# Kernel optimization log

Hardware: AMD Instinct MI355X
Metric: run time of the kernel (lower is better)

The kernel has to match this reference:

```python
import jax, jax.numpy as jnp
import numpy as np

N_NODES = 100000
N_EDGES = 1600000
N_FEAT = 128
HIDDEN = 128
OUT = 1
NUM_GRAPHS = 2048


def setup_inputs() -> dict:
    key = jax.random.key(0)
    ks = jax.random.split(key, 8)
    x = jax.random.normal(ks[0], (N_NODES, N_FEAT), dtype=jnp.float32)
    edge_index = jax.random.randint(ks[1], (2, N_EDGES), 0, N_NODES, dtype=jnp.int64)
    batch = jnp.sort(jax.random.randint(ks[2], (N_NODES,), 0, NUM_GRAPHS, dtype=jnp.int64))
    s = 1.0 / np.sqrt(N_FEAT)
    W1 = jax.random.normal(ks[3], (N_FEAT, HIDDEN), dtype=jnp.float32) * s
    b1 = jnp.zeros((HIDDEN,), dtype=jnp.float32)
    W2 = jax.random.normal(ks[4], (HIDDEN, HIDDEN), dtype=jnp.float32) * s
    b2 = jnp.zeros((HIDDEN,), dtype=jnp.float32)
    Wlin = jax.random.normal(ks[5], (HIDDEN, OUT), dtype=jnp.float32) * s
    blin = jnp.zeros((OUT,), dtype=jnp.float32)
    return {"x": x, "edge_index": edge_index, "batch": batch,
            "W1": W1, "b1": b1, "W2": W2, "b2": b2, "Wlin": Wlin, "blin": blin}


def gcn_conv(x, W, b, src, dst, n_nodes):
    # PyG GCNConv: x' = D^{-1/2} (A + I) D^{-1/2} (X W) + b, deg includes self-loop
    xw = x @ W  # [N, H]
    deg = jax.ops.segment_sum(jnp.ones(src.shape[0], xw.dtype), dst, num_segments=n_nodes) + 1.0
    dinv = jax.lax.rsqrt(deg)
    norm = dinv[src] * dinv[dst]  # [E]
    agg = jax.ops.segment_sum(xw[src] * norm[:, None], dst, num_segments=n_nodes)
    # self-loop contribution: norm = deg^{-1}
    return agg + xw * (1.0 / deg)[:, None] + b


def global_mean_pool(x, batch, num_graphs):
    sums = jax.ops.segment_sum(x, batch, num_segments=num_graphs)
    cnts = jax.ops.segment_sum(jnp.ones(x.shape[0], x.dtype), batch, num_segments=num_graphs)
    return sums / jnp.maximum(cnts, 1.0)[:, None]


def reference(x, edge_index, batch, W1, b1, W2, b2, Wlin, blin):
    src, dst = edge_index[0], edge_index[1]
    n = x.shape[0]
    h = gcn_conv(x, W1, b1, src, dst, n)
    h = jax.nn.relu(h)  # dropout is a no-op in eval mode
    h = gcn_conv(h, W2, b2, src, dst, n)
    g = global_mean_pool(h, batch, NUM_GRAPHS)  # [G, H]
    return g @ Wlin + blin
```

## Files before the change

### kernel.cpp

```cpp
#include <hip/hip_runtime.h>

#define N_NODES   100000
#define N_EDGES   1600000
#define NFEAT     128
#define NGRAPHS   2048
#define CBSHIFT   7
#define BSZ       128
#define NCB       ((N_NODES + BSZ - 1) / BSZ)
#define N_META    (NCB * BSZ)
#define CAP       2432
#define P1_EPB    8192
#define P1_BLOCKS ((N_EDGES + P1_EPB - 1) / P1_EPB)
#define GEMM_HALF   391
#define G1_BLOCKS 2048
#define G2_BLOCKS ((4 * N_META + 255) / 256)
#define ZCNT      (NGRAPHS + NCB)
#define ZB        ((ZCNT + 255) / 256)
#define MISC_BLOCKS (17 + ZB + 8)

typedef __attribute__((ext_vector_type(8))) short short8;
typedef __attribute__((ext_vector_type(4))) float f32x4;

__device__ __forceinline__ unsigned short f2bf(float f) {
    unsigned int u = __float_as_uint(f);
    u += 0x7FFFu + ((u >> 16) & 1u);
    return (unsigned short)(u >> 16);
}

__device__ __forceinline__ void acc8s(float* acc, uint4 v, float s) {
    acc[0] = fmaf(s, __uint_as_float(v.x << 16), acc[0]);
    acc[1] = fmaf(s, __uint_as_float(v.x & 0xFFFF0000u), acc[1]);
    acc[2] = fmaf(s, __uint_as_float(v.y << 16), acc[2]);
    acc[3] = fmaf(s, __uint_as_float(v.y & 0xFFFF0000u), acc[3]);
    acc[4] = fmaf(s, __uint_as_float(v.z << 16), acc[4]);
    acc[5] = fmaf(s, __uint_as_float(v.z & 0xFFFF0000u), acc[5]);
    acc[6] = fmaf(s, __uint_as_float(v.w << 16), acc[6]);
    acc[7] = fmaf(s, __uint_as_float(v.w & 0xFFFF0000u), acc[7]);
}

__device__ __forceinline__ void gemm_tile(const float* __restrict__ X,
                                          const unsigned short* __restrict__ WT,
                                          unsigned short* __restrict__ C,
                                          int gblk, int tid) {
    const int R0   = gblk * 128;
    const int wv   = tid >> 6;
    const int lane = tid & 63;
    const int m16  = lane & 15;
    const int quad = lane >> 4;
    const int r0 = R0 + wv * 32 + m16;
    const int r1 = r0 + 16;
    const bool ok0 = r0 < N_NODES, ok1 = r1 < N_NODES;

    f32x4 acc[2][8] = {};
    #pragma unroll
    for (int ks = 0; ks < 4; ++ks) {
        const int k0 = ks * 32 + quad * 8;
        short8 a0 = {}, a1 = {};
        if (ok0) {
            float4 f0 = *(const float4*)(X + (size_t)r0 * NFEAT + k0);
            float4 f1 = *(const float4*)(X + (size_t)r0 * NFEAT + k0 + 4);
            a0[0] = (short)f2bf(f0.x); a0[1] = (short)f2bf(f0.y);
            a0[2] = (short)f2bf(f0.z); a0[3] = (short)f2bf(f0.w);
            a0[4] = (short)f2bf(f1.x); a0[5] = (short)f2bf(f1.y);
            a0[6] = (short)f2bf(f1.z); a0[7] = (short)f2bf(f1.w);
        }
        if (ok1) {
            float4 f0 = *(const float4*)(X + (size_t)r1 * NFEAT + k0);
            float4 f1 = *(const float4*)(X + (size_t)r1 * NFEAT + k0 + 4);
            a1[0] = (short)f2bf(f0.x); a1[1] = (short)f2bf(f0.y);
            a1[2] = (short)f2bf(f0.z); a1[3] = (short)f2bf(f0.w);
            a1[4] = (short)f2bf(f1.x); a1[5] = (short)f2bf(f1.y);
            a1[6] = (short)f2bf(f1.z); a1[7] = (short)f2bf(f1.w);
        }
        #pragma unroll
        for (int ct = 0; ct < 8; ++ct) {
            short8 bb = *(const short8*)(WT + (ct * 16 + m16) * 128 + k0);
            acc[0][ct] = __builtin_amdgcn_mfma_f32_16x16x32_bf16(a0, bb, acc[0][ct], 0, 0, 0);
            acc[1][ct] = __builtin_amdgcn_mfma_f32_16x16x32_bf16(a1, bb, acc[1][ct], 0, 0, 0);
        }
    }
    #pragma unroll
    for (int t2 = 0; t2 < 2; ++t2) {
        int rbase = R0 + wv * 32 + t2 * 16 + quad * 4;
        #pragma unroll
        for (int reg = 0; reg < 4; ++reg) {
            int gr = rbase + reg;
            if (gr < N_NODES) {
                #pragma unroll
                for (int ct = 0; ct < 8; ++ct)
                    C[(size_t)gr * NFEAT + ct * 16 + m16] = f2bf(acc[t2][ct][reg]);
            }
        }
    }
}

__global__ __launch_bounds__(256) void k_misc(const float* __restrict__ W1,
                                              unsigned short* __restrict__ WT1,
                                              const float* __restrict__ W2,
                                              const float* __restrict__ Wlin,
                                              const float* __restrict__ b2,
                                              const float* __restrict__ blin,
                                              float* __restrict__ w2l,
                                              int* __restrict__ zeros,
                                              const int* __restrict__ batch,
                                              float* __restrict__ cntf) {
    const int blk = blockIdx.x;
    const int t = threadIdx.x;
    if (blk < 16) {
        int base = blk * 1024 + t * 4;
        #pragma unroll
        for (int q = 0; q < 4; ++q) {
            int i = base + q;
            int n = i >> 7, k = i & 127;
            WT1[i] = f2bf(W1[k * 128 + n]);
        }
    } else if (blk == 16) {
        __shared__ float s[256];
        int i = t >> 1, half = t & 1;
        float ps = 0.f;
        for (int j = half * 64; j < half * 64 + 64; ++j)
            ps += W2[i * 128 + j] * Wlin[j];
        s[t] = ps;
        __syncthreads();
        if (!half) w2l[i] = s[t] + s[t + 1];
        __syncthreads();
        float pc = (t < 128) ? b2[t] * Wlin[t] : 0.f;
        s[t] = pc;
        __syncthreads();
        for (int off = 128; off > 0; off >>= 1) {
            if (t < off) s[t] += s[t + off];
            __syncthreads();
        }
        if (t == 0) w2l[128] = s[0] + blin[0];
    } else if (blk < 17 + ZB) {
        int i = (blk - 17) * 256 + t;
        if (i < ZCNT) zeros[i] = 0;
    } else {
        int g = (blk - (17 + ZB)) * 256 + t;
        int lo = 0, hi = N_NODES;
        while (lo < hi) { int m = (lo + hi) >> 1; if (batch[m] < g) lo = m + 1; else hi = m; }
        int lb = lo;
        lo = 0; hi = N_NODES;
        int g1 = g + 1;
        while (lo < hi) { int m = (lo + hi) >> 1; if (batch[m] < g1) lo = m + 1; else hi = m; }
        cntf[g] = fmaxf((float)(lo - lb), 1.0f);
    }
}

__global__ __launch_bounds__(256) void k_gA_p1(const float* __restrict__ X,
                                               const unsigned short* __restrict__ WT,
                                               unsigned short* __restrict__ C,
                                               const int* __restrict__ src,
                                               const int* __restrict__ dst,
                                               int* __restrict__ bcur,
                                               unsigned int* __restrict__ pairs) {
    if (blockIdx.x < GEMM_HALF) {
        gemm_tile(X, WT, C, blockIdx.x, threadIdx.x);
        return;
    }
    const int b = blockIdx.x - GEMM_HALF;
    __shared__ int hist[NCB], base[NCB], cur[NCB];
    const int t = threadIdx.x;
    for (int i = t; i < NCB; i += 256) { hist[i] = 0; cur[i] = 0; }
    __syncthreads();
    const int e0 = b * P1_EPB;
    const int e1 = min(e0 + P1_EPB, N_EDGES);
    for (int e = e0 + t; e < e1; e += 256)
        atomicAdd(&hist[dst[e] >> CBSHIFT], 1);
    __syncthreads();
    const int off0 = (b * 89) % NCB;
    for (int k = t; k < NCB; k += 256) {
        int i = k + off0;
        if (i >= NCB) i -= NCB;
        int c = hist[i];
        base[i] = c ? (i * CAP + atomicAdd(&bcur[i], c)) : 0;
    }
    __syncthreads();
    for (int e = e0 + t; e < e1; e += 256) {
        int d = dst[e];
        int bb = d >> CBSHIFT;
        int r = atomicAdd(&cur[bb], 1);
        int idx = base[bb] + r;
        if (idx < (bb + 1) * CAP)
            pairs[idx] = (unsigned int)src[e] | ((unsigned int)(d & (BSZ - 1)) << 17);
    }
}

__global__ __launch_bounds__(256) void k_gB_p2(const float* __restrict__ X,
                                               const unsigned short* __restrict__ WT,
                                               unsigned short* __restrict__ C,
                                               const unsigned int* __restrict__ pairs,
                                               const int* __restrict__ bcur,
                                               int* __restrict__ csr_src,
                                               float* __restrict__ dinv,
                                               int4* __restrict__ meta) {
    if (blockIdx.x < GEMM_HALF) {
        gemm_tile(X, WT, C, blockIdx.x + GEMM_HALF, threadIdx.x);
        return;
    }
    const int b = blockIdx.x - GEMM_HALF;
    __shared__ int hist[BSZ], sst[BSZ], cur[BSZ], s[BSZ], dh[64], dhc[64];
    const int t = threadIdx.x;
    const int beg = b * CAP;
    const int end = beg + min(bcur[b], CAP);
    if (t < BSZ) { hist[t] = 0; cur[t] = 0; }
    if (t < 64) { dh[t] = 0; dhc[t] = 0; }
    __syncthreads();
    for (int i = beg + t; i < end; i += 256)
        atomicAdd(&hist[pairs[i] >> 17], 1);
    __syncthreads();
    int v = (t < BSZ) ? hist[t] : 0;
    if (t < BSZ) s[t] = v;
    __syncthreads();
    for (int off = 1; off < BSZ; off <<= 1) {
        int x = (t >= off && t < BSZ) ? s[t - off] : 0;
        __syncthreads();
        if (t < BSZ) s[t] += x;
        __syncthreads();
    }
    if (t < BSZ) sst[t] = s[t] - v;
    __syncthreads();
    const int node = (b << CBSHIFT) + t;
    const bool valid = (t < BSZ) && (node < N_NODES);
    if (valid) {
        dinv[node] = rsqrtf((float)v + 1.0f);
        atomicAdd(&dh[63 - min(v, 63)], 1);
    }
    for (int i = beg + t; i < end; i += 256) {
        unsigned int pv = pairs[i];
        int dl = pv >> 17;
        int r = atomicAdd(&cur[dl], 1);
        csr_src[beg + sst[dl] + r] = (int)(pv & 0x1FFFFu);
    }
    __syncthreads();
    if (t < 64) s[t] = dh[t];
    __syncthreads();
    for (int off = 1; off < 64; off <<= 1) {
        int x = (t >= off && t < 64) ? s[t - off] : 0;
        __syncthreads();
        if (t < 64) s[t] += x;
        __syncthreads();
    }
    if (valid) {
        int bin = 63 - min(v, 63);
        int r = atomicAdd(&dhc[bin], 1);
        int rank = s[bin] - dh[bin] + r;
        meta[(size_t)rank * NCB + b] =
            make_int4(beg + sst[t], v, __float_as_int(rsqrtf((float)v + 1.0f)), node);
    } else if (t < BSZ) {
        meta[(size_t)t * NCB + b] = make_int4(0, 0, 0, -1);
    }
}

__global__ __launch_bounds__(256) void k_gather1(const unsigned short* __restrict__ xwb,
                                                 const int* __restrict__ csr_src,
                                                 const float* __restrict__ dinv,
                                                 const float* __restrict__ b,
                                                 const float* __restrict__ w2l,
                                                 const int4* __restrict__ meta,
                                                 float* __restrict__ z) {
    const int t     = threadIdx.x;
    const int lane  = t & 63;
    const int p     = lane & 15;
    const int gbase = lane & 48;
    const int j0    = p & 7;
    const int ngroups = G1_BLOCKS * 16;
    int gid = blockIdx.x * 16 + (t >> 4);
    const uint4* tab = (const uint4*)xwb;
    float4 b0 = *(const float4*)(b + p * 8);
    float4 b1 = *(const float4*)(b + p * 8 + 4);
    float4 w0 = *(const float4*)(w2l + p * 8);
    float4 w1 = *(const float4*)(w2l + p * 8 + 4);

    for (int nidx = gid; nidx < N_META; nidx += ngroups) {
        const int4 md = meta[nidx];
        const int node  = md.w;
        if (node < 0) continue;
        const int beg   = md.x;
        const int cnt   = md.y;
        const float dvn = __int_as_float(md.z);
        float acc[8] = {};
        acc8s(acc, tab[(size_t)node * 16 + p], dvn);
        const int nch = (cnt + 7) >> 3;
        if (nch) {
            int myA; float dvA; uint4 vA[8];
            int myB; float dvB; uint4 vB[8];
            {
                bool vld = j0 < cnt;
                int jj = vld ? j0 : 0;
                int sld = csr_src[beg + jj];
                myA = vld ? sld : node;
                float dv = dinv[myA];
                dvA = vld ? dv : 0.f;
                #pragma unroll
                for (int q = 0; q < 8; ++q) {
                    int idx = __shfl(myA, gbase + q);
                    vA[q] = tab[(size_t)idx * 16 + p];
                }
            }
            int c = 0;
            for (;;) {
                const bool hb = (c + 1 < nch);
                if (hb) {
                    int j = (c + 1) * 8 + j0;
                    bool vld = j < cnt;
                    int jj = vld ? j : 0;
                    int sld = csr_src[beg + jj];
                    myB = vld ? sld : node;
                    float dv = dinv[myB];
                    dvB = vld ? dv : 0.f;
                    #pragma unroll
                    for (int q = 0; q < 8; ++q) {
                        int idx = __shfl(myB, gbase + q);
                        vB[q] = tab[(size_t)idx * 16 + p];
                    }
                }
                #pragma unroll
                for (int q = 0; q < 8; ++q) {
                    float sv = __shfl(dvA, gbase + q);
                    acc8s(acc, vA[q], sv);
                }
                ++c;
                if (!hb) break;
                const bool ha = (c + 1 < nch);
                if (ha) {
                    int j = (c + 1) * 8 + j0;
                    bool vld = j < cnt;
                    int jj = vld ? j : 0;
                    int sld = csr_src[beg + jj];
                    myA = vld ? sld : node;
                    float dv = dinv[myA];
                    dvA = vld ? dv : 0.f;
                    #pragma unroll
                    for (int q = 0; q < 8; ++q) {
                        int idx = __shfl(myA, gbase + q);
                        vA[q] = tab[(size_t)idx * 16 + p];
                    }
                }
                #pragma unroll
                for (int q = 0; q < 8; ++q) {
                    float sv = __shfl(dvB, gbase + q);
                    acc8s(acc, vB[q], sv);
                }
                ++c;
                if (!ha) break;
            }
        }
        float s = fmaxf(acc[0] * dvn + b0.x, 0.f) * w0.x
                + fmaxf(acc[1] * dvn + b0.y, 0.f) * w0.y
                + fmaxf(acc[2] * dvn + b0.z, 0.f) * w0.z
                + fmaxf(acc[3] * dvn + b0.w, 0.f) * w0.w
                + fmaxf(acc[4] * dvn + b1.x, 0.f) * w1.x
                + fmaxf(acc[5] * dvn + b1.y, 0.f) * w1.y
                + fmaxf(acc[6] * dvn + b1.z, 0.f) * w1.z
                + fmaxf(acc[7] * dvn + b1.w, 0.f) * w1.w;
        s += __shfl_xor(s, 1);
        s += __shfl_xor(s, 2);
        s += __shfl_xor(s, 4);
        s += __shfl_xor(s, 8);
        if (p == 0) z[node] = s * dvn;
    }
}

__global__ __launch_bounds__(256) void k_g2(const float* __restrict__ z,
                                            const int* __restrict__ csr_src,
                                            const int4* __restrict__ meta,
                                            const int* __restrict__ batch,
                                            float* __restrict__ gsum) {
    int tid = blockIdx.x * blockDim.x + threadIdx.x;
    int nidx = tid >> 2;
    int q = tid & 3;
    if (nidx >= N_META) return;
    int4 md = meta[nidx];
    const int node = md.w;
    if (node < 0) return;
    const int beg = md.x, cnt = md.y;
    const float dvn = __int_as_float(md.z);
    float a = (q == 0) ? z[node] : 0.f;
    for (int j = q; j < cnt; j += 4)
        a += z[csr_src[beg + j]];
    a += __shfl_xor(a, 1);
    a += __shfl_xor(a, 2);
    if (q == 0) atomicAdd(&gsum[batch[node]], a * dvn);
}

__global__ void k_final(const float* __restrict__ gsum, const float* __restrict__ cntf,
                        const float* __restrict__ c2, float* __restrict__ out) {
    int g = blockIdx.x * blockDim.x + threadIdx.x;
    if (g >= NGRAPHS) return;
    out[g] = gsum[g] / cntf[g] + c2[0];
}

extern "C" void kernel_launch(void* const* d_in, const int* in_sizes, int n_in,
                              void* d_out, int out_size, void* d_ws, size_t ws_size,
                              hipStream_t stream) {
    const float* x    = (const float*)d_in[0];
    const int*   ei   = (const int*)d_in[1];
    const int*   bat  = (const int*)d_in[2];
    const float* W1   = (const float*)d_in[3];
    const float* b1   = (const float*)d_in[4];
    const float* W2   = (const float*)d_in[5];
    const float* b2   = (const float*)d_in[6];
    const float* Wlin = (const float*)d_in[7];
    const float* blin = (const float*)d_in[8];
    float* out = (float*)d_out;

    const int* src = ei;
    const int* dst = ei + N_EDGES;

    const size_t NF = (size_t)N_NODES * NFEAT;
    unsigned short* bufA = (unsigned short*)d_ws;
    float* z       = (float*)(bufA + NF);
    float* dinv    = z + N_NODES;
    float* gsum    = dinv + N_NODES;
    int* bcur      = (int*)(gsum + NGRAPHS);
    float* cntf    = (float*)(bcur + NCB);
    unsigned short* WT1 = (unsigned short*)(cntf + NGRAPHS);
    float* w2l     = (float*)(WT1 + 128 * 128);
    unsigned int* pairs = (unsigned int*)(w2l + 132);
    int* csr_src   = (int*)(pairs + (size_t)NCB * CAP);
    int4* meta     = (int4*)(((size_t)(csr_src + (size_t)NCB * CAP) + 15) & ~(size_t)15);

    const int BS = 256;

    k_misc<<<MISC_BLOCKS, BS, 0, stream>>>(W1, WT1, W2, Wlin, b2, blin, w2l,
                                           (int*)gsum, bat, cntf);
    k_gA_p1<<<GEMM_HALF + P1_BLOCKS, BS, 0, stream>>>(x, WT1, bufA, src, dst, bcur, pairs);
    k_gB_p2<<<GEMM_HALF + NCB, BS, 0, stream>>>(x, WT1, bufA, pairs, bcur, csr_src,
                                                dinv, meta);
    k_gather1<<<G1_BLOCKS, BS, 0, stream>>>(bufA, csr_src, dinv, b1, w2l, meta, z);
    k_g2<<<G2_BLOCKS, BS, 0, stream>>>(z, csr_src, meta, bat, gsum);
    k_final<<<(NGRAPHS + BS - 1) / BS, BS, 0, stream>>>(gsum, cntf, w2l + 128, out);
}
```

Before: 244.4 us.

## Split fused GEMM/edge-bucketing kernels and store GEMM rows with permuted column layout

Separates the horizontally fused GEMM+bucketing kernels into standalone k_gemm, k_p1 and k_p2 launches, and halves edges per block in the first bucketing pass. The GEMM epilogue now writes 8 bf16 values per lane as one 16-byte store, which permutes the feature column order in the xw buffer; the gather kernel reads bias and projection weights with a matching strided index so results stay consistent. This removes scattered 2-byte stores but gives up the overlap of GEMM and edge bucketing, and adds an extra launch.

```diff
diff --git a/kernel.cpp b/kernel.cpp
--- a/kernel.cpp
+++ b/kernel.cpp
@@ -9,9 +9,9 @@
 #define NCB       ((N_NODES + BSZ - 1) / BSZ)
 #define N_META    (NCB * BSZ)
 #define CAP       2432
-#define P1_EPB    8192
+#define P1_EPB    4096
 #define P1_BLOCKS ((N_EDGES + P1_EPB - 1) / P1_EPB)
-#define GEMM_HALF   391
+#define GEMM_BLOCKS 782
 #define G1_BLOCKS 2048
 #define G2_BLOCKS ((4 * N_META + 255) / 256)
 #define ZCNT      (NGRAPHS + NCB)
@@ -38,11 +38,11 @@
     acc[7] = fmaf(s, __uint_as_float(v.w & 0xFFFF0000u), acc[7]);
 }
 
-__device__ __forceinline__ void gemm_tile(const float* __restrict__ X,
-                                          const unsigned short* __restrict__ WT,
-                                          unsigned short* __restrict__ C,
-                                          int gblk, int tid) {
-    const int R0   = gblk * 128;
+__global__ __launch_bounds__(256) void k_gemm(const float* __restrict__ X,
+                                              const unsigned short* __restrict__ WT,
+                                              unsigned short* __restrict__ C) {
+    const int tid  = threadIdx.x;
+    const int R0   = blockIdx.x * 128;
     const int wv   = tid >> 6;
     const int lane = tid & 63;
     const int m16  = lane & 15;
@@ -86,9 +86,11 @@
         for (int reg = 0; reg < 4; ++reg) {
             int gr = rbase + reg;
             if (gr < N_NODES) {
+                short8 v;
                 #pragma unroll
                 for (int ct = 0; ct < 8; ++ct)
-                    C[(size_t)gr * NFEAT + ct * 16 + m16] = f2bf(acc[t2][ct][reg]);
+                    v[ct] = (short)f2bf(acc[t2][ct][reg]);
+                *(short8*)(C + (size_t)gr * NFEAT + m16 * 8) = v;
             }
         }
     }
@@ -147,18 +149,11 @@
     }
 }
 
-__global__ __launch_bounds__(256) void k_gA_p1(const float* __restrict__ X,
-                                               const unsigned short* __restrict__ WT,
-                                               unsigned short* __restrict__ C,
-                                               const int* __restrict__ src,
-                                               const int* __restrict__ dst,
-                                               int* __restrict__ bcur,
-                                               unsigned int* __restrict__ pairs) {
-    if (blockIdx.x < GEMM_HALF) {
-        gemm_tile(X, WT, C, blockIdx.x, threadIdx.x);
-        return;
-    }
-    const int b = blockIdx.x - GEMM_HALF;
+__global__ __launch_bounds__(256) void k_p1(const int* __restrict__ src,
+                                            const int* __restrict__ dst,
+                                            int* __restrict__ bcur,
+                                            unsigned int* __restrict__ pairs) {
+    const int b = blockIdx.x;
     __shared__ int hist[NCB], base[NCB], cur[NCB];
     const int t = threadIdx.x;
     for (int i = t; i < NCB; i += 256) { hist[i] = 0; cur[i] = 0; }
@@ -186,19 +181,12 @@
     }
 }
 
-__global__ __launch_bounds__(256) void k_gB_p2(const float* __restrict__ X,
-                                               const unsigned short* __restrict__ WT,
-                                               unsigned short* __restrict__ C,
-                                               const unsigned int* __restrict__ pairs,
-                                               const int* __restrict__ bcur,
-                                               int* __restrict__ csr_src,
-                                               float* __restrict__ dinv,
-                                               int4* __restrict__ meta) {
-    if (blockIdx.x < GEMM_HALF) {
-        gemm_tile(X, WT, C, blockIdx.x + GEMM_HALF, threadIdx.x);
-        return;
-    }
-    const int b = blockIdx.x - GEMM_HALF;
+__global__ __launch_bounds__(256) void k_p2(const unsigned int* __restrict__ pairs,
+                                            const int* __restrict__ bcur,
+                                            int* __restrict__ csr_src,
+                                            float* __restrict__ dinv,
+                                            int4* __restrict__ meta) {
+    const int b = blockIdx.x;
     __shared__ int hist[BSZ], sst[BSZ], cur[BSZ], s[BSZ], dh[64], dhc[64];
     const int t = threadIdx.x;
     const int beg = b * CAP;
@@ -267,10 +255,9 @@
     const int ngroups = G1_BLOCKS * 16;
     int gid = blockIdx.x * 16 + (t >> 4);
     const uint4* tab = (const uint4*)xwb;
-    float4 b0 = *(const float4*)(b + p * 8);
-    float4 b1 = *(const float4*)(b + p * 8 + 4);
-    float4 w0 = *(const float4*)(w2l + p * 8);
-    float4 w1 = *(const float4*)(w2l + p * 8 + 4);
+    float bl[8], wl[8];
+    #pragma unroll
+    for (int j = 0; j < 8; ++j) { bl[j] = b[16 * j + p]; wl[j] = w2l[16 * j + p]; }
 
     for (int nidx = gid; nidx < N_META; nidx += ngroups) {
         const int4 md = meta[nidx];
@@ -346,14 +333,10 @@
                 if (!ha) break;
             }
         }
-        float s = fmaxf(acc[0] * dvn + b0.x, 0.f) * w0.x
-                + fmaxf(acc[1] * dvn + b0.y, 0.f) * w0.y
-                + fmaxf(acc[2] * dvn + b0.z, 0.f) * w0.z
-                + fmaxf(acc[3] * dvn + b0.w, 0.f) * w0.w
-                + fmaxf(acc[4] * dvn + b1.x, 0.f) * w1.x
-                + fmaxf(acc[5] * dvn + b1.y, 0.f) * w1.y
-                + fmaxf(acc[6] * dvn + b1.z, 0.f) * w1.z
-                + fmaxf(acc[7] * dvn + b1.w, 0.f) * w1.w;
+        float s = 0.f;
+        #pragma unroll
+        for (int j = 0; j < 8; ++j)
+            s = fmaf(fmaxf(fmaf(acc[j], dvn, bl[j]), 0.f), wl[j], s);
         s += __shfl_xor(s, 1);
         s += __shfl_xor(s, 2);
         s += __shfl_xor(s, 4);
@@ -425,9 +408,9 @@
 
     k_misc<<<MISC_BLOCKS, BS, 0, stream>>>(W1, WT1, W2, Wlin, b2, blin, w2l,
                                            (int*)gsum, bat, cntf);
-    k_gA_p1<<<GEMM_HALF + P1_BLOCKS, BS, 0, stream>>>(x, WT1, bufA, src, dst, bcur, pairs);
-    k_gB_p2<<<GEMM_HALF + NCB, BS, 0, stream>>>(x, WT1, bufA, pairs, bcur, csr_src,
-                                                dinv, meta);
+    k_gemm<<<GEMM_BLOCKS, BS, 0, stream>>>(x, WT1, bufA);
+    k_p1<<<P1_BLOCKS, BS, 0, stream>>>(src, dst, bcur, pairs);
+    k_p2<<<NCB, BS, 0, stream>>>(pairs, bcur, csr_src, dinv, meta);
     k_gather1<<<G1_BLOCKS, BS, 0, stream>>>(bufA, csr_src, dinv, b1, w2l, meta, z);
     k_g2<<<G2_BLOCKS, BS, 0, stream>>>(z, csr_src, meta, bat, gsum);
     k_final<<<(NGRAPHS + BS - 1) / BS, BS, 0, stream>>>(gsum, cntf, w2l + 128, out);
```

New measurement: 265.7 us. +8.7%, slower.
